# Kernel tuning notes

Hardware: AMD Instinct MI355X
Metric: run time of the kernel (lower is better)

## Reference

```python
import jax, jax.numpy as jnp
import numpy as np

BETA_MEM = 0.9
BETA_INH = 0.6
THRESHOLD = 1.0  # snn.Leaky default


def setup_inputs() -> dict:
    key = jax.random.key(0)
    k1, = jax.random.split(key, 1)
    T, B = 1024, 16384
    spike_seq = (jax.random.uniform(k1, (T, B, 2)) < 0.05).astype(jnp.float32)
    w_exc = jnp.array([[0.7, 1.0]], dtype=jnp.float32)  # fc_exc.weight, [1, 2]
    w_inh = jnp.array(-1.0, dtype=jnp.float32)          # scalar inhibitory weight
    return {"spike_seq": spike_seq, "w_exc": w_exc, "w_inh": w_inh}


@jax.custom_vjp
def spike_fn(x):
    # Heaviside spike with ATan surrogate gradient (snntorch default, alpha=2)
    return (x > 0).astype(x.dtype)

def _spike_fwd(x):
    return spike_fn(x), x

def _spike_bwd(x, g):
    return (g / (1.0 + (jnp.pi * x) ** 2),)

spike_fn.defvjp(_spike_fwd, _spike_bwd)


def reference(spike_seq, w_exc, w_inh):
    T, B, _ = spike_seq.shape
    mem0 = jnp.zeros((B, 1), dtype=spike_seq.dtype)
    inh0 = jnp.zeros((B, 1), dtype=spike_seq.dtype)

    def step(carry, x_t):
        mem, inh = carry
        cur_exc = x_t @ w_exc.T                      # [B, 1]
        fm1 = x_t[:, 0:1]                            # [B, 1]
        inh = BETA_INH * inh + fm1
        cur = cur_exc + w_inh * inh
        # snn.Leaky: reset (subtract) computed from previous mem, detached
        reset = jax.lax.stop_gradient((mem - THRESHOLD > 0).astype(mem.dtype))
        mem = BETA_MEM * mem + cur - reset * THRESHOLD
        spk = spike_fn(mem - THRESHOLD)
        return (mem, inh), (spk, mem)

    _, (spk_rec, mem_rec) = jax.lax.scan(step, (mem0, inh0), spike_seq)
    return spk_rec, mem_rec  # each [T, B, 1]
```

## Files before the change

### kernel.cpp

```cpp
#include <hip/hip_runtime.h>

#define T_LEN   1024
#define B_N     16384
#define PH      16
#define NPHASES (T_LEN / PH)

__shared__ __align__(16) float2 IN_lds[4][PH][64];
__shared__ __align__(16) float2 OUT_lds[2][PH][64];

static __device__ __forceinline__ void block_barrier() {
  asm volatile("" ::: "memory");
  __builtin_amdgcn_s_barrier();
  asm volatile("" ::: "memory");
}

__global__ __launch_bounds__(192, 1) void FMFMNeuronInhib_34033320854098_kernel(
    const float* __restrict__ x,
    const float* __restrict__ w_exc,
    const float* __restrict__ w_inh,
    float* __restrict__ out) {
#pragma clang fp contract(off)
  const int lane = threadIdx.x & 63;
  const int wid  = threadIdx.x >> 6;
  const int nb0  = blockIdx.x * 64;

  float* __restrict__ spk_out = out;
  float* __restrict__ mem_out = out + (size_t)T_LEN * B_N;

  if (wid == 1) {
    const int half = lane >> 5;
    const int l32  = lane & 31;
    auto issue_phase = [&](int q) {
#pragma unroll
      for (int j = 0; j < 8; ++j) {
        const int t = q * PH + 2 * j + half;
        const float* src = x + ((size_t)t * B_N + nb0) * 2 + (size_t)l32 * 4;
        __builtin_amdgcn_global_load_lds(
            (const __attribute__((address_space(1))) void*)src,
            (__attribute__((address_space(3))) void*)&IN_lds[q & 3][2 * j][0],
            16, 0, 0);
      }
    };
    issue_phase(0); issue_phase(1); issue_phase(2);
    asm volatile("s_waitcnt vmcnt(16)" ::: "memory");
    block_barrier();
    for (int p = 0; p < NPHASES; ++p) {
      if (p + 3 < NPHASES) issue_phase(p + 3);
      if (p <= NPHASES - 4)      asm volatile("s_waitcnt vmcnt(16)" ::: "memory");
      else if (p == NPHASES - 3) asm volatile("s_waitcnt vmcnt(8)"  ::: "memory");
      else                       asm volatile("s_waitcnt vmcnt(0)"  ::: "memory");
      block_barrier();
    }
  } else if (wid == 0) {
    const float w0 = w_exc[0];
    const float w1 = w_exc[1];
    const float wi = w_inh[0];
    float mem = 0.0f, inh = 0.0f;
    block_barrier();
    for (int p = 0; p < NPHASES; ++p) {
      float2 xv[PH];
#pragma unroll
      for (int u = 0; u < PH; ++u) xv[u] = IN_lds[p & 3][u][lane];
#pragma unroll
      for (int u = 0; u < PH; ++u) {
        const float x0 = xv[u].x;
        const float x1 = xv[u].y;
        const float cur_exc = x0 * w0 + x1 * w1;
        inh = 0.6f * inh + x0;
        const float cur = cur_exc + wi * inh;
        const float reset = (mem > 1.0f) ? 1.0f : 0.0f;
        mem = 0.9f * mem + cur - reset;
        const float spk = (mem > 1.0f) ? 1.0f : 0.0f;
        OUT_lds[p & 1][u][lane] = make_float2(spk, mem);
      }
      asm volatile("s_waitcnt lgkmcnt(0)" ::: "memory");
      block_barrier();
    }
  } else {
    block_barrier();
    for (int p = 0; p < NPHASES; ++p) {
      if (p >= 1) {
        const int tb = (p - 1) * PH;
#pragma unroll
        for (int u = 0; u < PH; ++u) {
          const float2 v = OUT_lds[(p - 1) & 1][u][lane];
          const size_t idx = (size_t)(tb + u) * B_N + nb0 + lane;
          spk_out[idx] = v.x;
          mem_out[idx] = v.y;
        }
        asm volatile("s_waitcnt lgkmcnt(0)" ::: "memory");
      }
      block_barrier();
    }
    const int tb = (NPHASES - 1) * PH;
#pragma unroll
    for (int u = 0; u < PH; ++u) {
      const float2 v = OUT_lds[(NPHASES - 1) & 1][u][lane];
      const size_t idx = (size_t)(tb + u) * B_N + nb0 + lane;
      spk_out[idx] = v.x;
      mem_out[idx] = v.y;
    }
  }
}

extern "C" void kernel_launch(void* const* d_in, const int* in_sizes, int n_in,
                              void* d_out, int out_size, void* d_ws, size_t ws_size,
                              hipStream_t stream) {
  const float* x     = (const float*)d_in[0];
  const float* w_exc = (const float*)d_in[1];
  const float* w_inh = (const float*)d_in[2];
  float* out = (float*)d_out;

  dim3 grid(B_N / 64);
  dim3 block(192);
  hipLaunchKernelGGL(FMFMNeuronInhib_34033320854098_kernel, grid, block, 0, stream,
                     x, w_exc, w_inh, out);
}
```

Measured before the change: 230.9 us.

## Split output LDS into spike/mem planes and drain with two float4 store waves

The interleaved float2 output staging buffer becomes separate spike and membrane planes. A fourth wave is added so one wave writes spikes and another writes membrane values. Each writer now uses 16-byte float4 LDS reads and global stores instead of per-lane scalar stores. The aim is to raise store throughput and overlap the output write stream with the compute wave, at the cost of an extra wave per block and a larger block.

```diff
diff --git a/kernel.cpp b/kernel.cpp
--- a/kernel.cpp
+++ b/kernel.cpp
@@ -1,12 +1,15 @@
 #include <hip/hip_runtime.h>
 
-#define T_LEN   1024
-#define B_N     16384
-#define PH      16
-#define NPHASES (T_LEN / PH)
+#define T_LEN 1024
+#define B_N   16384
+#define PH    16
+#define NPH   (T_LEN / PH)
+#define RIN   4
 
-__shared__ __align__(16) float2 IN_lds[4][PH][64];
-__shared__ __align__(16) float2 OUT_lds[2][PH][64];
+
+__shared__ __align__(16) float2 IN_lds[RIN][PH][64];
+__shared__ __align__(16) float  SPK_lds[2][PH][64];
+__shared__ __align__(16) float  MEM_lds[2][PH][64];
 
 static __device__ __forceinline__ void block_barrier() {
   asm volatile("" ::: "memory");
@@ -14,7 +17,7 @@
   asm volatile("" ::: "memory");
 }
 
-__global__ __launch_bounds__(192, 1) void FMFMNeuronInhib_34033320854098_kernel(
+__global__ __launch_bounds__(256, 1) void FMFMNeuronInhib_34033320854098_kernel(
     const float* __restrict__ x,
     const float* __restrict__ w_exc,
     const float* __restrict__ w_inh,
@@ -44,11 +47,11 @@
     issue_phase(0); issue_phase(1); issue_phase(2);
     asm volatile("s_waitcnt vmcnt(16)" ::: "memory");
     block_barrier();
-    for (int p = 0; p < NPHASES; ++p) {
-      if (p + 3 < NPHASES) issue_phase(p + 3);
-      if (p <= NPHASES - 4)      asm volatile("s_waitcnt vmcnt(16)" ::: "memory");
-      else if (p == NPHASES - 3) asm volatile("s_waitcnt vmcnt(8)"  ::: "memory");
-      else                       asm volatile("s_waitcnt vmcnt(0)"  ::: "memory");
+    for (int p = 0; p < NPH; ++p) {
+      if (p + 3 < NPH) issue_phase(p + 3);
+      if (p <= NPH - 4)      asm volatile("s_waitcnt vmcnt(16)" ::: "memory");
+      else if (p == NPH - 3) asm volatile("s_waitcnt vmcnt(8)"  ::: "memory");
+      else                   asm volatile("s_waitcnt vmcnt(0)"  ::: "memory");
       block_barrier();
     }
   } else if (wid == 0) {
@@ -57,7 +60,7 @@
     const float wi = w_inh[0];
     float mem = 0.0f, inh = 0.0f;
     block_barrier();
-    for (int p = 0; p < NPHASES; ++p) {
+    for (int p = 0; p < NPH; ++p) {
       float2 xv[PH];
 #pragma unroll
       for (int u = 0; u < PH; ++u) xv[u] = IN_lds[p & 3][u][lane];
@@ -71,35 +74,35 @@
         const float reset = (mem > 1.0f) ? 1.0f : 0.0f;
         mem = 0.9f * mem + cur - reset;
         const float spk = (mem > 1.0f) ? 1.0f : 0.0f;
-        OUT_lds[p & 1][u][lane] = make_float2(spk, mem);
+        SPK_lds[p & 1][u][lane] = spk;
+        MEM_lds[p & 1][u][lane] = mem;
       }
       asm volatile("s_waitcnt lgkmcnt(0)" ::: "memory");
       block_barrier();
     }
   } else {
+    const float* plane = (wid == 2) ? &SPK_lds[0][0][0] : &MEM_lds[0][0][0];
+    float* gout        = (wid == 2) ? spk_out : mem_out;
+    const int r  = lane >> 4;
+    const int n0 = (lane & 15) * 4;
+    auto drain = [&](int p) {
+      const int tb   = p * PH;
+      const int slot = p & 1;
+#pragma unroll
+      for (int j = 0; j < 4; ++j) {
+        const int row = 4 * j + r;
+        const float4 v =
+            *(const float4*)(plane + ((size_t)slot * PH + row) * 64 + n0);
+        *(float4*)&gout[(size_t)(tb + row) * B_N + nb0 + n0] = v;
+      }
+      asm volatile("s_waitcnt lgkmcnt(0)" ::: "memory");
+    };
     block_barrier();
-    for (int p = 0; p < NPHASES; ++p) {
-      if (p >= 1) {
-        const int tb = (p - 1) * PH;
-#pragma unroll
-        for (int u = 0; u < PH; ++u) {
-          const float2 v = OUT_lds[(p - 1) & 1][u][lane];
-          const size_t idx = (size_t)(tb + u) * B_N + nb0 + lane;
-          spk_out[idx] = v.x;
-          mem_out[idx] = v.y;
-        }
-        asm volatile("s_waitcnt lgkmcnt(0)" ::: "memory");
-      }
+    for (int p = 0; p < NPH; ++p) {
+      if (p >= 1) drain(p - 1);
       block_barrier();
     }
-    const int tb = (NPHASES - 1) * PH;
-#pragma unroll
-    for (int u = 0; u < PH; ++u) {
-      const float2 v = OUT_lds[(NPHASES - 1) & 1][u][lane];
-      const size_t idx = (size_t)(tb + u) * B_N + nb0 + lane;
-      spk_out[idx] = v.x;
-      mem_out[idx] = v.y;
-    }
+    drain(NPH - 1);
   }
 }
 
@@ -112,7 +115,7 @@
   float* out = (float*)d_out;
 
   dim3 grid(B_N / 64);
-  dim3 block(192);
+  dim3 block(256);
   hipLaunchKernelGGL(FMFMNeuronInhib_34033320854098_kernel, grid, block, 0, stream,
                      x, w_exc, w_inh, out);
 }
```

New measurement: 229.5 us. About the same (-0.6%).
